# Optimization experiments

Hardware: AMD Instinct MI355X
Metric: run time of the kernel (lower is better)

The kernel has to match this reference:

```python
import jax, jax.numpy as jnp
import numpy as np

T, B, S = 32, 32, 64
I = H = C = 1024  # input_size == hidden_size required by the original module's wiring
A = 128           # attention_size


def setup_inputs() -> dict:
    key = jax.random.key(0)
    ks = jax.random.split(key, 10)
    s_ih = 1.0 / np.sqrt(H)
    s_a = 1.0 / np.sqrt(H + C)
    return {
        "inputs": jax.random.normal(ks[0], (T, B, I), jnp.float32),
        "context": jax.random.normal(ks[1], (S, B, C), jnp.float32),
        # LSTMCell params (PyTorch layout: gates ordered i, f, g, o)
        "W_ih": jax.random.normal(ks[2], (4 * H, I), jnp.float32) * s_ih,
        "W_hh": jax.random.normal(ks[3], (4 * H, H), jnp.float32) * s_ih,
        "b_ih": jax.random.normal(ks[4], (4 * H,), jnp.float32) * s_ih,
        "b_hh": jax.random.normal(ks[5], (4 * H,), jnp.float32) * s_ih,
        # Attention params: linear1 [A, H+C], linear2 [1, A]
        "W1": jax.random.normal(ks[6], (A, H + C), jnp.float32) * s_a,
        "b1": jax.random.normal(ks[7], (A,), jnp.float32) * s_a,
        "W2": jax.random.normal(ks[8], (1, A), jnp.float32) * (1.0 / np.sqrt(A)),
        "b2": jax.random.normal(ks[9], (1,), jnp.float32) * (1.0 / np.sqrt(A)),
    }


def reference(inputs, context, W_ih, W_hh, b_ih, b_hh, W1, b1, W2, b2):
    Tn, Bn, _ = inputs.shape
    Hn = W_hh.shape[1]
    xt = jnp.transpose(context, (1, 0, 2))  # [B, S, C]
    # Split linear1 weight into hidden-part and context-part so the
    # context projection can be hoisted out of the time loop (same math
    # as concatenating [y, xt] then applying linear1).
    W1_y = W1[:, :Hn]          # [A, H]
    W1_x = W1[:, Hn:]          # [A, C]
    ctx_proj = jnp.einsum('bsc,ac->bsa', xt, W1_x)  # [B, S, A]
    bias = b_ih + b_hh

    def step(carry, x_t):
        h, c = carry
        gates = x_t @ W_ih.T + h @ W_hh.T + bias   # [B, 4H]
        i, f, g, o = jnp.split(gates, 4, axis=-1)
        c_new = jax.nn.sigmoid(f) * c + jax.nn.sigmoid(i) * jnp.tanh(g)
        h_new = jax.nn.sigmoid(o) * jnp.tanh(c_new)
        # additive attention: linear1 (no nonlinearity in original) -> linear2 -> softmax
        hid = h_new[:, None, :] @ W1_y.T[None] + ctx_proj + b1  # [B, S, A]
        scores = jnp.einsum('bsa,a->bs', hid, W2[0]) + b2[0]    # [B, S]
        attn = jax.nn.softmax(scores, axis=-1)
        weighted = jnp.einsum('bs,bsc->bc', attn, xt)           # [B, C]
        return (h_new, c_new), (weighted, attn)

    h0 = jnp.zeros((Bn, Hn), inputs.dtype)
    (h, c), (outputs, attentions) = jax.lax.scan(step, (h0, h0), inputs)
    return outputs, h, c, attentions
```

## Files before the change

### kernel.cpp

```cpp
#include <hip/hip_runtime.h>

#define T_ 32
#define B_ 32
#define S_ 64
#define C_ 1024
#define H_ 1024
#define NWG 64
#define HSLOT 32768

typedef __attribute__((ext_vector_type(8))) short bf16x8;
typedef __attribute__((ext_vector_type(4))) float f32x4;

#define OUT_H   1048576
#define OUT_CC  1081344
#define OUT_AT  1114112

__device__ __forceinline__ ushort f2b(float f) {
  unsigned u = __float_as_uint(f);
  unsigned r = (u + 0x7FFFu + ((u >> 16) & 1u)) >> 16;
  return (ushort)r;
}
__device__ __forceinline__ float b2f(ushort h) {
  return __uint_as_float(((unsigned)h) << 16);
}

__global__ __launch_bounds__(256) void k_init(const float* __restrict__ inp, ushort* __restrict__ inpb,
                                              const float* __restrict__ Wih, ushort* __restrict__ Wihb,
                                              const float* __restrict__ Whh, ushort* __restrict__ Whhb,
                                              const float* __restrict__ W1, const float* __restrict__ W2,
                                              const float* __restrict__ bih, const float* __restrict__ bhh,
                                              float* __restrict__ v, float* __restrict__ bias,
                                              ushort* __restrict__ hring, unsigned* __restrict__ flags) {
  int blk = blockIdx.x, tid = threadIdx.x;
  if (blk < 4608) {
    const float* src; ushort* dst; int base;
    if (blk < 512) { src = inp; dst = inpb; base = blk; }
    else if (blk < 2560) { src = Wih; dst = Wihb; base = blk - 512; }
    else { src = Whh; dst = Whhb; base = blk - 2560; }
    size_t i = ((size_t)base * 256 + tid) * 8;
    float4 v0 = *reinterpret_cast<const float4*>(src + i);
    float4 v1 = *reinterpret_cast<const float4*>(src + i + 4);
    uint4 o;
    o.x = (unsigned)f2b(v0.x) | ((unsigned)f2b(v0.y) << 16);
    o.y = (unsigned)f2b(v0.z) | ((unsigned)f2b(v0.w) << 16);
    o.z = (unsigned)f2b(v1.x) | ((unsigned)f2b(v1.y) << 16);
    o.w = (unsigned)f2b(v1.z) | ((unsigned)f2b(v1.w) << 16);
    *reinterpret_cast<uint4*>(dst + i) = o;
  } else if (blk < 4612) {
    int c = (blk - 4608) * 256 + tid;
    float acc = 0.f;
#pragma unroll 8
    for (int a = 0; a < 128; ++a) acc += W1[a * 2048 + 1024 + c] * W2[a];
    v[c] = acc;
  } else if (blk < 4628) {
    int jj = (blk - 4612) * 256 + tid;
    bias[jj] = bih[jj] + bhh[jj];
  } else if (blk < 4632) {
    unsigned* hz = reinterpret_cast<unsigned*>(hring);
    int base = (blk - 4628) * 4096;
    for (int i = 0; i < 16; ++i) hz[base + i * 256 + tid] = 0u;
  } else {
    for (int i = 0; i < 4; ++i) flags[i * 256 + tid] = 0u;
  }
}

__global__ __launch_bounds__(1024, 4) void k_rec(const ushort* __restrict__ Whhb, const ushort* __restrict__ Wihb,
                                                 const ushort* __restrict__ inpb, ushort* __restrict__ hring,
                                                 const float* __restrict__ ctx, const float* __restrict__ v,
                                                 const float* __restrict__ bias,
                                                 float* __restrict__ out, unsigned* __restrict__ flags) {
  int tid = threadIdx.x, lane = tid & 63, w = tid >> 6;
  int wg = blockIdx.x;

  __shared__ uint4 hl4[4096];
  __shared__ float red[4][4][16][32];
  __shared__ __align__(16) ushort hs[32][16];
  __shared__ float v_s[1024];
  __shared__ float sc_s[64];
  __shared__ float att_s[64];

  if (wg >= NWG) {
    int b = wg - NWG;
    v_s[tid] = v[tid];
    __syncthreads();
    {
      int s = w * 4;
#pragma unroll
      for (int si = 0; si < 4; ++si, ++s) {
        const float* xr = ctx + (size_t)(s * B_ + b) * C_;
        float acc = 0.f;
#pragma unroll
        for (int i = 0; i < 16; ++i) { int c = lane + i * 64; acc += xr[c] * v_s[c]; }
        for (int off = 32; off; off >>= 1) acc += __shfl_down(acc, off);
        if (lane == 0) sc_s[s] = acc;
      }
    }
    __syncthreads();
    if (tid < 64) {
      float val = sc_s[tid];
      float mx = val;
      for (int off = 32; off; off >>= 1) mx = fmaxf(mx, __shfl_xor(mx, off));
      float e = expf(val - mx);
      float sm = e;
      for (int off = 32; off; off >>= 1) sm += __shfl_xor(sm, off);
      att_s[tid] = e / sm;
    }
    __syncthreads();
    if (tid < 256) {
      const float4* ctx4 = reinterpret_cast<const float4*>(ctx);
      float4 a4 = {0.f, 0.f, 0.f, 0.f};
      for (int s = 0; s < 64; ++s) {
        float a = att_s[s];
        float4 x = ctx4[(size_t)(s * B_ + b) * 256 + tid];
        a4.x += a * x.x; a4.y += a * x.y; a4.z += a * x.z; a4.w += a * x.w;
      }
#pragma unroll 4
      for (int t = 0; t < T_; ++t)
        reinterpret_cast<float4*>(out + (size_t)(t * B_ + b) * C_)[tid] = a4;
    }
    if (tid < 64) {
      float av = att_s[tid];
#pragma unroll 4
      for (int t = 0; t < T_; ++t) out[OUT_AT + (t * B_ + b) * 64 + tid] = av;
    }
    return;
  }

  int q = w & 3, ks = w >> 2;
  int g = lane >> 4, r = lane & 15;
  int hidx0 = wg * 16 + q * 4;
  int kbase = ks * 256;
  int j = (r >> 2) * 1024 + hidx0 + (r & 3);
  bf16x8 ah[8], ax[8];
  {
    const ushort* ap = Whhb + (size_t)j * 1024 + kbase + g * 8;
    const ushort* axp = Wihb + (size_t)j * 1024 + kbase + g * 8;
#pragma unroll
    for (int kk = 0; kk < 8; ++kk) {
      ah[kk] = *reinterpret_cast<const bf16x8*>(ap + kk * 32);
      ax[kk] = *reinterpret_cast<const bf16x8*>(axp + kk * 32);
    }
  }
  float c_reg = 0.f;
  int eb = tid & 31, hl = (tid >> 5) & 3, qq = tid >> 7;
  int ehidx = wg * 16 + qq * 4 + hl;
  float bs_i = 0.f, bs_f = 0.f, bs_g = 0.f, bs_o = 0.f;
  if (tid < 512) {
    bs_i = bias[ehidx];
    bs_f = bias[1024 + ehidx];
    bs_g = bias[2048 + ehidx];
    bs_o = bias[3072 + ehidx];
  }
  int cb = ks * 32 + g;

#pragma unroll 1
  for (int t = 0; t < T_; ++t) {
    {
      const uint4* s4 = reinterpret_cast<const uint4*>(inpb + (size_t)t * HSLOT);
      uint4 v0 = s4[tid], v1 = s4[tid + 1024], v2 = s4[tid + 2048], v3 = s4[tid + 3072];
      int c0 = tid, c1 = tid + 1024, c2 = tid + 2048, c3 = tid + 3072;
      hl4[(c0 >> 7) * 128 + ((c0 & 127) ^ ((c0 >> 7) & 7))] = v0;
      hl4[(c1 >> 7) * 128 + ((c1 & 127) ^ ((c1 >> 7) & 7))] = v1;
      hl4[(c2 >> 7) * 128 + ((c2 & 127) ^ ((c2 >> 7) & 7))] = v2;
      hl4[(c3 >> 7) * 128 + ((c3 & 127) ^ ((c3 >> 7) & 7))] = v3;
    }
    __syncthreads();
    f32x4 acc0 = (f32x4)(0.f), acc1 = (f32x4)(0.f);
#pragma unroll
    for (int kk = 0; kk < 8; ++kk) {
      int c16 = cb + kk * 4;
      bf16x8 b0 = *reinterpret_cast<const bf16x8*>(&hl4[r * 128 + (c16 ^ (r & 7))]);
      bf16x8 b1 = *reinterpret_cast<const bf16x8*>(&hl4[(r + 16) * 128 + (c16 ^ (r & 7))]);
      acc0 = __builtin_amdgcn_mfma_f32_16x16x32_bf16(ax[kk], b0, acc0, 0, 0, 0);
      acc1 = __builtin_amdgcn_mfma_f32_16x16x32_bf16(ax[kk], b1, acc1, 0, 0, 0);
    }
    if (t > 0 && w == 0) {
      for (;;) {
        unsigned vfl = __hip_atomic_load(&flags[lane * 16], __ATOMIC_RELAXED, __HIP_MEMORY_SCOPE_AGENT);
        if (__all((int)(vfl >= (unsigned)t))) break;
        __builtin_amdgcn_s_sleep(1);
      }
    }
    __syncthreads();
    {
      const uint4* s4 = reinterpret_cast<const uint4*>(hring + (size_t)t * HSLOT);
      uint4 v0 = s4[tid], v1 = s4[tid + 1024], v2 = s4[tid + 2048], v3 = s4[tid + 3072];
      int c0 = tid, c1 = tid + 1024, c2 = tid + 2048, c3 = tid + 3072;
      hl4[(c0 >> 7) * 128 + ((c0 & 127) ^ ((c0 >> 7) & 7))] = v0;
      hl4[(c1 >> 7) * 128 + ((c1 & 127) ^ ((c1 >> 7) & 7))] = v1;
      hl4[(c2 >> 7) * 128 + ((c2 & 127) ^ ((c2 >> 7) & 7))] = v2;
      hl4[(c3 >> 7) * 128 + ((c3 & 127) ^ ((c3 >> 7) & 7))] = v3;
    }
    __syncthreads();
#pragma unroll
    for (int kk = 0; kk < 8; ++kk) {
      int c16 = cb + kk * 4;
      bf16x8 b0 = *reinterpret_cast<const bf16x8*>(&hl4[r * 128 + (c16 ^ (r & 7))]);
      bf16x8 b1 = *reinterpret_cast<const bf16x8*>(&hl4[(r + 16) * 128 + (c16 ^ (r & 7))]);
      acc0 = __builtin_amdgcn_mfma_f32_16x16x32_bf16(ah[kk], b0, acc0, 0, 0, 0);
      acc1 = __builtin_amdgcn_mfma_f32_16x16x32_bf16(ah[kk], b1, acc1, 0, 0, 0);
    }
#pragma unroll
    for (int e = 0; e < 4; ++e) {
      red[q][ks][g * 4 + e][r] = acc0[e];
      red[q][ks][g * 4 + e][r + 16] = acc1[e];
    }
    __syncthreads();
    if (tid < 512) {
      float ig = red[qq][0][0 + hl][eb]  + red[qq][1][0 + hl][eb]  + red[qq][2][0 + hl][eb]  + red[qq][3][0 + hl][eb]  + bs_i;
      float fg = red[qq][0][4 + hl][eb]  + red[qq][1][4 + hl][eb]  + red[qq][2][4 + hl][eb]  + red[qq][3][4 + hl][eb]  + bs_f;
      float gg = red[qq][0][8 + hl][eb]  + red[qq][1][8 + hl][eb]  + red[qq][2][8 + hl][eb]  + red[qq][3][8 + hl][eb]  + bs_g;
      float og = red[qq][0][12 + hl][eb] + red[qq][1][12 + hl][eb] + red[qq][2][12 + hl][eb] + red[qq][3][12 + hl][eb] + bs_o;
      float si = 1.f / (1.f + __expf(-ig));
      float sf = 1.f / (1.f + __expf(-fg));
      float so = 1.f / (1.f + __expf(-og));
      float c_new = sf * c_reg + si * tanhf(gg);
      float h_new = so * tanhf(c_new);
      c_reg = c_new;
      hs[eb][qq * 4 + hl] = f2b(h_new);
      if (t == T_ - 1) {
        out[OUT_H + eb * 1024 + ehidx] = h_new;
        out[OUT_CC + eb * 1024 + ehidx] = c_new;
      }
    }
    __syncthreads();
    if (t != T_ - 1 && w == 0) {
      ushort* hout = hring + (size_t)(t + 1) * HSLOT;
      int b = lane >> 1, half = lane & 1;
      uint4 vv = *reinterpret_cast<const uint4*>(&hs[b][half * 8]);
      unsigned* hp = reinterpret_cast<unsigned*>(hout) + b * 512 + wg * 8 + half * 4;
      __hip_atomic_store(hp + 0, vv.x, __ATOMIC_RELAXED, __HIP_MEMORY_SCOPE_AGENT);
      __hip_atomic_store(hp + 1, vv.y, __ATOMIC_RELAXED, __HIP_MEMORY_SCOPE_AGENT);
      __hip_atomic_store(hp + 2, vv.z, __ATOMIC_RELAXED, __HIP_MEMORY_SCOPE_AGENT);
      __hip_atomic_store(hp + 3, vv.w, __ATOMIC_RELAXED, __HIP_MEMORY_SCOPE_AGENT);
      asm volatile("s_waitcnt vmcnt(0)" ::: "memory");
      if (lane == 0)
        __hip_atomic_store(&flags[wg * 16], (unsigned)(t + 1), __ATOMIC_RELAXED, __HIP_MEMORY_SCOPE_AGENT);
    }
  }
}

extern "C" void kernel_launch(void* const* d_in, const int* in_sizes, int n_in,
                              void* d_out, int out_size, void* d_ws, size_t ws_size,
                              hipStream_t stream) {
  const float* inp = (const float*)d_in[0];
  const float* ctx = (const float*)d_in[1];
  const float* Wih = (const float*)d_in[2];
  const float* Whh = (const float*)d_in[3];
  const float* bih = (const float*)d_in[4];
  const float* bhh = (const float*)d_in[5];
  const float* W1  = (const float*)d_in[6];
  const float* W2  = (const float*)d_in[8];
  float* out = (float*)d_out;
  char* wsb = (char*)d_ws;

  float* v     = (float*)(wsb + 0);
  float* bias  = (float*)(wsb + 4096);
  ushort* hring = (ushort*)(wsb + 32768);
  ushort* inpb = (ushort*)(wsb + 2195456);
  ushort* Wihb = (ushort*)(wsb + 4292608);
  ushort* Whhb = (ushort*)(wsb + 12681216);
  unsigned* flags = (unsigned*)(wsb + 21069824);

  hipLaunchKernelGGL(k_init, dim3(4633), dim3(256), 0, stream,
                     inp, inpb, Wih, Wihb, Whh, Whhb, W1, W2, bih, bhh, v, bias, hring, flags);

  const ushort* Whhb_c = Whhb;
  const ushort* Wihb_c = Wihb;
  const ushort* inpb_c = inpb;
  const float* ctx_c = ctx;
  const float* v_c = v;
  const float* bias_c = bias;
  void* kargs[9];
  kargs[0] = (void*)&Whhb_c;
  kargs[1] = (void*)&Wihb_c;
  kargs[2] = (void*)&inpb_c;
  kargs[3] = (void*)&hring;
  kargs[4] = (void*)&ctx_c;
  kargs[5] = (void*)&v_c;
  kargs[6] = (void*)&bias_c;
  kargs[7] = (void*)&out;
  kargs[8] = (void*)&flags;
  hipLaunchCooperativeKernel((const void*)k_rec, dim3(NWG + 32), dim3(1024), kargs, 0, stream);
}
```

Measured before the change: 198.0 us.

## Replicate LSTM recurrence per XCD and precompute input projection upfront

The recurrence now runs as 8 independent replicas, one per XCD, each with 32 workgroups owning 32 hidden units. Workgroups get their rank by atomically counting on the XCD id, and each replica keeps its own hidden-state ring, so per-step flag polling and h exchange stay within one XCD's L2. The x·W_ih^T projection for all timesteps is hoisted into a prologue that writes a bf16 buffer, and the weight-to-bf16 conversion moves into k_rec, which drops it from k_init. This should shorten the serial per-step critical path, at the cost of redundant recurrence work across the replicas and a dependence on the hardware scheduler placing exactly 32 blocks on each XCD.

```diff
diff --git a/kernel.cpp b/kernel.cpp
--- a/kernel.cpp
+++ b/kernel.cpp
@@ -5,8 +5,8 @@
 #define S_ 64
 #define C_ 1024
 #define H_ 1024
-#define NWG 64
 #define HSLOT 32768
+#define NXCD 8
 
 typedef __attribute__((ext_vector_type(8))) short bf16x8;
 typedef __attribute__((ext_vector_type(4))) float f32x4;
@@ -25,138 +25,209 @@
 }
 
 __global__ __launch_bounds__(256) void k_init(const float* __restrict__ inp, ushort* __restrict__ inpb,
-                                              const float* __restrict__ Wih, ushort* __restrict__ Wihb,
-                                              const float* __restrict__ Whh, ushort* __restrict__ Whhb,
                                               const float* __restrict__ W1, const float* __restrict__ W2,
                                               const float* __restrict__ bih, const float* __restrict__ bhh,
                                               float* __restrict__ v, float* __restrict__ bias,
                                               ushort* __restrict__ hring, unsigned* __restrict__ flags) {
   int blk = blockIdx.x, tid = threadIdx.x;
-  if (blk < 4608) {
-    const float* src; ushort* dst; int base;
-    if (blk < 512) { src = inp; dst = inpb; base = blk; }
-    else if (blk < 2560) { src = Wih; dst = Wihb; base = blk - 512; }
-    else { src = Whh; dst = Whhb; base = blk - 2560; }
-    size_t i = ((size_t)base * 256 + tid) * 8;
-    float4 v0 = *reinterpret_cast<const float4*>(src + i);
-    float4 v1 = *reinterpret_cast<const float4*>(src + i + 4);
+  if (blk < 512) {
+    size_t i = ((size_t)blk * 256 + tid) * 8;
+    float4 v0 = *reinterpret_cast<const float4*>(inp + i);
+    float4 v1 = *reinterpret_cast<const float4*>(inp + i + 4);
     uint4 o;
     o.x = (unsigned)f2b(v0.x) | ((unsigned)f2b(v0.y) << 16);
     o.y = (unsigned)f2b(v0.z) | ((unsigned)f2b(v0.w) << 16);
     o.z = (unsigned)f2b(v1.x) | ((unsigned)f2b(v1.y) << 16);
     o.w = (unsigned)f2b(v1.z) | ((unsigned)f2b(v1.w) << 16);
-    *reinterpret_cast<uint4*>(dst + i) = o;
-  } else if (blk < 4612) {
-    int c = (blk - 4608) * 256 + tid;
+    *reinterpret_cast<uint4*>(inpb + i) = o;
+  } else if (blk < 516) {
+    int c = (blk - 512) * 256 + tid;
     float acc = 0.f;
 #pragma unroll 8
     for (int a = 0; a < 128; ++a) acc += W1[a * 2048 + 1024 + c] * W2[a];
     v[c] = acc;
-  } else if (blk < 4628) {
-    int jj = (blk - 4612) * 256 + tid;
+  } else if (blk < 532) {
+    int jj = (blk - 516) * 256 + tid;
     bias[jj] = bih[jj] + bhh[jj];
-  } else if (blk < 4632) {
-    unsigned* hz = reinterpret_cast<unsigned*>(hring);
-    int base = (blk - 4628) * 4096;
-    for (int i = 0; i < 16; ++i) hz[base + i * 256 + tid] = 0u;
+  } else if (blk < 564) {
+    int base = (blk - 532) * 4096;
+    for (int i = 0; i < 16; ++i) {
+      int idx = base + i * 256 + tid;
+      int xcd = idx >> 14, off = idx & 16383;
+      reinterpret_cast<unsigned*>(hring + (size_t)xcd * 33 * HSLOT)[off] = 0u;
+    }
   } else {
-    for (int i = 0; i < 4; ++i) flags[i * 256 + tid] = 0u;
-  }
-}
-
-__global__ __launch_bounds__(1024, 4) void k_rec(const ushort* __restrict__ Whhb, const ushort* __restrict__ Wihb,
+    for (int i = 0; i < 17; ++i) {
+      int idx = i * 256 + tid;
+      if (idx < 4104) flags[idx] = 0u;
+    }
+  }
+}
+
+__global__ __launch_bounds__(1024, 4) void k_rec(const float* __restrict__ Wih, const float* __restrict__ Whh,
                                                  const ushort* __restrict__ inpb, ushort* __restrict__ hring,
                                                  const float* __restrict__ ctx, const float* __restrict__ v,
-                                                 const float* __restrict__ bias,
-                                                 float* __restrict__ out, unsigned* __restrict__ flags) {
+                                                 const float* __restrict__ bias, float* __restrict__ out,
+                                                 unsigned* __restrict__ flags, ushort* __restrict__ xpT) {
   int tid = threadIdx.x, lane = tid & 63, w = tid >> 6;
-  int wg = blockIdx.x;
-
   __shared__ uint4 hl4[4096];
-  __shared__ float red[4][4][16][32];
-  __shared__ __align__(16) ushort hs[32][16];
+  __shared__ float red[8][2][17][33];
   __shared__ float v_s[1024];
   __shared__ float sc_s[64];
   __shared__ float att_s[64];
-
-  if (wg >= NWG) {
-    int b = wg - NWG;
-    v_s[tid] = v[tid];
-    __syncthreads();
-    {
-      int s = w * 4;
-#pragma unroll
-      for (int si = 0; si < 4; ++si, ++s) {
-        const float* xr = ctx + (size_t)(s * B_ + b) * C_;
-        float acc = 0.f;
-#pragma unroll
-        for (int i = 0; i < 16; ++i) { int c = lane + i * 64; acc += xr[c] * v_s[c]; }
-        for (int off = 32; off; off >>= 1) acc += __shfl_down(acc, off);
-        if (lane == 0) sc_s[s] = acc;
-      }
-    }
-    __syncthreads();
-    if (tid < 64) {
-      float val = sc_s[tid];
-      float mx = val;
-      for (int off = 32; off; off >>= 1) mx = fmaxf(mx, __shfl_xor(mx, off));
-      float e = expf(val - mx);
-      float sm = e;
-      for (int off = 32; off; off >>= 1) sm += __shfl_xor(sm, off);
-      att_s[tid] = e / sm;
-    }
-    __syncthreads();
-    if (tid < 256) {
-      const float4* ctx4 = reinterpret_cast<const float4*>(ctx);
-      float4 a4 = {0.f, 0.f, 0.f, 0.f};
-      for (int s = 0; s < 64; ++s) {
-        float a = att_s[s];
-        float4 x = ctx4[(size_t)(s * B_ + b) * 256 + tid];
-        a4.x += a * x.x; a4.y += a * x.y; a4.z += a * x.z; a4.w += a * x.w;
-      }
+  __shared__ float4 wgt_s[32];
+  __shared__ unsigned rank_s;
+
+  unsigned xcd;
+  asm volatile("s_getreg_b32 %0, hwreg(HW_REG_XCC_ID)" : "=s"(xcd));
+  xcd &= 7u;
+  if (tid == 0) rank_s = atomicAdd(&flags[4096 + xcd], 1u) & 31u;
+  __syncthreads();
+  int rank = (int)rank_s;
+  int hid0 = rank * 32;
+  ushort* hring_x = hring + (size_t)xcd * 33 * HSLOT;
+
+  v_s[tid] = v[tid];
+  __syncthreads();
+  {
+    int s = w * 4;
+#pragma unroll
+    for (int si = 0; si < 4; ++si, ++s) {
+      const float* xr = ctx + (size_t)(s * B_ + rank) * C_;
+      float acc = 0.f;
+#pragma unroll
+      for (int i = 0; i < 16; ++i) { int c = lane + i * 64; acc += xr[c] * v_s[c]; }
+      for (int off = 32; off; off >>= 1) acc += __shfl_down(acc, off);
+      if (lane == 0) sc_s[s] = acc;
+    }
+  }
+  __syncthreads();
+  if (tid < 64) {
+    float val = sc_s[tid];
+    float mx = val;
+    for (int off = 32; off; off >>= 1) mx = fmaxf(mx, __shfl_xor(mx, off));
+    float e = expf(val - mx);
+    float sm = e;
+    for (int off = 32; off; off >>= 1) sm += __shfl_xor(sm, off);
+    att_s[tid] = e / sm;
+  }
+  __syncthreads();
+  if (tid < 32) {
+    const float4* ctx4 = reinterpret_cast<const float4*>(ctx);
+    float4 a4 = {0.f, 0.f, 0.f, 0.f};
+    for (int s = 0; s < 64; ++s) {
+      float a = att_s[s];
+      float4 x = ctx4[(size_t)(s * B_ + rank) * 256 + xcd * 32 + tid];
+      a4.x += a * x.x; a4.y += a * x.y; a4.z += a * x.z; a4.w += a * x.w;
+    }
+    wgt_s[tid] = a4;
+  }
+  __syncthreads();
+  {
+    int t = tid >> 5, c4 = tid & 31;
+    reinterpret_cast<float4*>(out)[(size_t)(t * B_ + rank) * 256 + xcd * 32 + c4] = wgt_s[c4];
+  }
+  if (tid < 64) {
+    float av = att_s[tid];
 #pragma unroll 4
-      for (int t = 0; t < T_; ++t)
-        reinterpret_cast<float4*>(out + (size_t)(t * B_ + b) * C_)[tid] = a4;
-    }
-    if (tid < 64) {
-      float av = att_s[tid];
-#pragma unroll 4
-      for (int t = 0; t < T_; ++t) out[OUT_AT + (t * B_ + b) * 64 + tid] = av;
-    }
-    return;
-  }
-
-  int q = w & 3, ks = w >> 2;
+    for (int t = 0; t < T_; ++t) out[OUT_AT + (t * B_ + rank) * 64 + tid] = av;
+  }
+
+  int tq = w >> 1, ks = w & 1;
   int g = lane >> 4, r = lane & 15;
-  int hidx0 = wg * 16 + q * 4;
-  int kbase = ks * 256;
-  int j = (r >> 2) * 1024 + hidx0 + (r & 3);
-  bf16x8 ah[8], ax[8];
+  int jrow = (r >> 2) * 1024 + hid0 + tq * 4 + (r & 3);
+
+  int eb = tid >> 5, ehl = tid & 31;
+  int ehidx = hid0 + ehl;
+  int etq = ehl >> 2, er = ehl & 3;
+
   {
-    const ushort* ap = Whhb + (size_t)j * 1024 + kbase + g * 8;
-    const ushort* axp = Wihb + (size_t)j * 1024 + kbase + g * 8;
-#pragma unroll
-    for (int kk = 0; kk < 8; ++kk) {
-      ah[kk] = *reinterpret_cast<const bf16x8*>(ap + kk * 32);
-      ax[kk] = *reinterpret_cast<const bf16x8*>(axp + kk * 32);
-    }
-  }
+    bf16x8 ax[16];
+    const float* ap = Wih + (size_t)jrow * 1024 + ks * 512 + g * 8;
+#pragma unroll
+    for (int kk = 0; kk < 16; ++kk) {
+      float4 f0 = *reinterpret_cast<const float4*>(ap + kk * 32);
+      float4 f1 = *reinterpret_cast<const float4*>(ap + kk * 32 + 4);
+      bf16x8 t8;
+      t8[0] = (short)f2b(f0.x); t8[1] = (short)f2b(f0.y);
+      t8[2] = (short)f2b(f0.z); t8[3] = (short)f2b(f0.w);
+      t8[4] = (short)f2b(f1.x); t8[5] = (short)f2b(f1.y);
+      t8[6] = (short)f2b(f1.z); t8[7] = (short)f2b(f1.w);
+      ax[kk] = t8;
+    }
+#pragma unroll 1
+    for (int mc = 0; mc < 32; ++mc) {
+      __syncthreads();
+      {
+        const uint4* s4 = reinterpret_cast<const uint4*>(inpb + (size_t)mc * HSLOT);
+        uint4 v0 = s4[tid], v1 = s4[tid + 1024], v2 = s4[tid + 2048], v3 = s4[tid + 3072];
+        int c0 = tid, c1 = tid + 1024, c2 = tid + 2048, c3 = tid + 3072;
+        hl4[(c0 >> 7) * 128 + ((c0 & 127) ^ ((c0 >> 7) & 7))] = v0;
+        hl4[(c1 >> 7) * 128 + ((c1 & 127) ^ ((c1 >> 7) & 7))] = v1;
+        hl4[(c2 >> 7) * 128 + ((c2 & 127) ^ ((c2 >> 7) & 7))] = v2;
+        hl4[(c3 >> 7) * 128 + ((c3 & 127) ^ ((c3 >> 7) & 7))] = v3;
+      }
+      __syncthreads();
+      f32x4 a0 = (f32x4)(0.f), a1 = (f32x4)(0.f);
+#pragma unroll
+      for (int kk = 0; kk < 16; ++kk) {
+        int c16 = ks * 64 + kk * 4 + g;
+        bf16x8 b0 = *reinterpret_cast<const bf16x8*>(&hl4[r * 128 + (c16 ^ (r & 7))]);
+        bf16x8 b1 = *reinterpret_cast<const bf16x8*>(&hl4[(r + 16) * 128 + (c16 ^ (r & 7))]);
+        a0 = __builtin_amdgcn_mfma_f32_16x16x32_bf16(ax[kk], b0, a0, 0, 0, 0);
+        a1 = __builtin_amdgcn_mfma_f32_16x16x32_bf16(ax[kk], b1, a1, 0, 0, 0);
+      }
+#pragma unroll
+      for (int e = 0; e < 4; ++e) {
+        red[tq][ks][g * 4 + e][r] = a0[e];
+        red[tq][ks][g * 4 + e][r + 16] = a1[e];
+      }
+      __syncthreads();
+      {
+        int m = mc * 32 + eb;
+        ushort4 xv;
+        xv.x = f2b(red[etq][0][er][eb]      + red[etq][1][er][eb]);
+        xv.y = f2b(red[etq][0][4 + er][eb]  + red[etq][1][4 + er][eb]);
+        xv.z = f2b(red[etq][0][8 + er][eb]  + red[etq][1][8 + er][eb]);
+        xv.w = f2b(red[etq][0][12 + er][eb] + red[etq][1][12 + er][eb]);
+        *reinterpret_cast<ushort4*>(xpT + ((size_t)m * 1024 + ehidx) * 4) = xv;
+      }
+    }
+    asm volatile("s_waitcnt vmcnt(0)" ::: "memory");
+    __syncthreads();
+  }
+
+  bf16x8 ah[16];
+  {
+    const float* ap = Whh + (size_t)jrow * 1024 + ks * 512 + g * 8;
+#pragma unroll
+    for (int kk = 0; kk < 16; ++kk) {
+      float4 f0 = *reinterpret_cast<const float4*>(ap + kk * 32);
+      float4 f1 = *reinterpret_cast<const float4*>(ap + kk * 32 + 4);
+      bf16x8 t8;
+      t8[0] = (short)f2b(f0.x); t8[1] = (short)f2b(f0.y);
+      t8[2] = (short)f2b(f0.z); t8[3] = (short)f2b(f0.w);
+      t8[4] = (short)f2b(f1.x); t8[5] = (short)f2b(f1.y);
+      t8[6] = (short)f2b(f1.z); t8[7] = (short)f2b(f1.w);
+      ah[kk] = t8;
+    }
+  }
+
+  float bs0 = bias[ehidx], bs1 = bias[1024 + ehidx], bs2 = bias[2048 + ehidx], bs3 = bias[3072 + ehidx];
   float c_reg = 0.f;
-  int eb = tid & 31, hl = (tid >> 5) & 3, qq = tid >> 7;
-  int ehidx = wg * 16 + qq * 4 + hl;
-  float bs_i = 0.f, bs_f = 0.f, bs_g = 0.f, bs_o = 0.f;
-  if (tid < 512) {
-    bs_i = bias[ehidx];
-    bs_f = bias[1024 + ehidx];
-    bs_g = bias[2048 + ehidx];
-    bs_o = bias[3072 + ehidx];
-  }
-  int cb = ks * 32 + g;
 
 #pragma unroll 1
   for (int t = 0; t < T_; ++t) {
+    if (t > 0 && w == 0) {
+      for (;;) {
+        unsigned vf = __hip_atomic_load(&flags[(xcd * 32 + (lane & 31)) * 16], __ATOMIC_RELAXED, __HIP_MEMORY_SCOPE_AGENT);
+        if (__all((int)(vf >= (unsigned)t))) break;
+        __builtin_amdgcn_s_sleep(1);
+      }
+    }
+    __syncthreads();
     {
-      const uint4* s4 = reinterpret_cast<const uint4*>(inpb + (size_t)t * HSLOT);
+      const uint4* s4 = reinterpret_cast<const uint4*>(hring_x + (size_t)t * HSLOT);
       uint4 v0 = s4[tid], v1 = s4[tid + 1024], v2 = s4[tid + 2048], v3 = s4[tid + 3072];
       int c0 = tid, c1 = tid + 1024, c2 = tid + 2048, c3 = tid + 3072;
       hl4[(c0 >> 7) * 128 + ((c0 & 127) ^ ((c0 >> 7) & 7))] = v0;
@@ -165,78 +236,45 @@
       hl4[(c3 >> 7) * 128 + ((c3 & 127) ^ ((c3 >> 7) & 7))] = v3;
     }
     __syncthreads();
-    f32x4 acc0 = (f32x4)(0.f), acc1 = (f32x4)(0.f);
-#pragma unroll
-    for (int kk = 0; kk < 8; ++kk) {
-      int c16 = cb + kk * 4;
+    f32x4 a0 = (f32x4)(0.f), a1 = (f32x4)(0.f);
+#pragma unroll
+    for (int kk = 0; kk < 16; ++kk) {
+      int c16 = ks * 64 + kk * 4 + g;
       bf16x8 b0 = *reinterpret_cast<const bf16x8*>(&hl4[r * 128 + (c16 ^ (r & 7))]);
       bf16x8 b1 = *reinterpret_cast<const bf16x8*>(&hl4[(r + 16) * 128 + (c16 ^ (r & 7))]);
-      acc0 = __builtin_amdgcn_mfma_f32_16x16x32_bf16(ax[kk], b0, acc0, 0, 0, 0);
-      acc1 = __builtin_amdgcn_mfma_f32_16x16x32_bf16(ax[kk], b1, acc1, 0, 0, 0);
-    }
-    if (t > 0 && w == 0) {
-      for (;;) {
-        unsigned vfl = __hip_atomic_load(&flags[lane * 16], __ATOMIC_RELAXED, __HIP_MEMORY_SCOPE_AGENT);
-        if (__all((int)(vfl >= (unsigned)t))) break;
-        __builtin_amdgcn_s_sleep(1);
-      }
+      a0 = __builtin_amdgcn_mfma_f32_16x16x32_bf16(ah[kk], b0, a0, 0, 0, 0);
+      a1 = __builtin_amdgcn_mfma_f32_16x16x32_bf16(ah[kk], b1, a1, 0, 0, 0);
+    }
+#pragma unroll
+    for (int e = 0; e < 4; ++e) {
+      red[tq][ks][g * 4 + e][r] = a0[e];
+      red[tq][ks][g * 4 + e][r + 16] = a1[e];
     }
     __syncthreads();
     {
-      const uint4* s4 = reinterpret_cast<const uint4*>(hring + (size_t)t * HSLOT);
-      uint4 v0 = s4[tid], v1 = s4[tid + 1024], v2 = s4[tid + 2048], v3 = s4[tid + 3072];
-      int c0 = tid, c1 = tid + 1024, c2 = tid + 2048, c3 = tid + 3072;
-      hl4[(c0 >> 7) * 128 + ((c0 & 127) ^ ((c0 >> 7) & 7))] = v0;
-      hl4[(c1 >> 7) * 128 + ((c1 & 127) ^ ((c1 >> 7) & 7))] = v1;
-      hl4[(c2 >> 7) * 128 + ((c2 & 127) ^ ((c2 >> 7) & 7))] = v2;
-      hl4[(c3 >> 7) * 128 + ((c3 & 127) ^ ((c3 >> 7) & 7))] = v3;
-    }
-    __syncthreads();
-#pragma unroll
-    for (int kk = 0; kk < 8; ++kk) {
-      int c16 = cb + kk * 4;
-      bf16x8 b0 = *reinterpret_cast<const bf16x8*>(&hl4[r * 128 + (c16 ^ (r & 7))]);
-      bf16x8 b1 = *reinterpret_cast<const bf16x8*>(&hl4[(r + 16) * 128 + (c16 ^ (r & 7))]);
-      acc0 = __builtin_amdgcn_mfma_f32_16x16x32_bf16(ah[kk], b0, acc0, 0, 0, 0);
-      acc1 = __builtin_amdgcn_mfma_f32_16x16x32_bf16(ah[kk], b1, acc1, 0, 0, 0);
-    }
-#pragma unroll
-    for (int e = 0; e < 4; ++e) {
-      red[q][ks][g * 4 + e][r] = acc0[e];
-      red[q][ks][g * 4 + e][r + 16] = acc1[e];
-    }
-    __syncthreads();
-    if (tid < 512) {
-      float ig = red[qq][0][0 + hl][eb]  + red[qq][1][0 + hl][eb]  + red[qq][2][0 + hl][eb]  + red[qq][3][0 + hl][eb]  + bs_i;
-      float fg = red[qq][0][4 + hl][eb]  + red[qq][1][4 + hl][eb]  + red[qq][2][4 + hl][eb]  + red[qq][3][4 + hl][eb]  + bs_f;
-      float gg = red[qq][0][8 + hl][eb]  + red[qq][1][8 + hl][eb]  + red[qq][2][8 + hl][eb]  + red[qq][3][8 + hl][eb]  + bs_g;
-      float og = red[qq][0][12 + hl][eb] + red[qq][1][12 + hl][eb] + red[qq][2][12 + hl][eb] + red[qq][3][12 + hl][eb] + bs_o;
+      int m = t * 32 + eb;
+      ushort4 xv = *reinterpret_cast<const ushort4*>(xpT + ((size_t)m * 1024 + ehidx) * 4);
+      float ig = red[etq][0][er][eb]      + red[etq][1][er][eb]      + b2f(xv.x) + bs0;
+      float fg = red[etq][0][4 + er][eb]  + red[etq][1][4 + er][eb]  + b2f(xv.y) + bs1;
+      float gg = red[etq][0][8 + er][eb]  + red[etq][1][8 + er][eb]  + b2f(xv.z) + bs2;
+      float og = red[etq][0][12 + er][eb] + red[etq][1][12 + er][eb] + b2f(xv.w) + bs3;
       float si = 1.f / (1.f + __expf(-ig));
       float sf = 1.f / (1.f + __expf(-fg));
       float so = 1.f / (1.f + __expf(-og));
       float c_new = sf * c_reg + si * tanhf(gg);
       float h_new = so * tanhf(c_new);
       c_reg = c_new;
-      hs[eb][qq * 4 + hl] = f2b(h_new);
-      if (t == T_ - 1) {
+      if (t < T_ - 1) {
+        hring_x[(size_t)(t + 1) * HSLOT + eb * 1024 + ehidx] = f2b(h_new);
+      } else {
         out[OUT_H + eb * 1024 + ehidx] = h_new;
         out[OUT_CC + eb * 1024 + ehidx] = c_new;
       }
     }
-    __syncthreads();
-    if (t != T_ - 1 && w == 0) {
-      ushort* hout = hring + (size_t)(t + 1) * HSLOT;
-      int b = lane >> 1, half = lane & 1;
-      uint4 vv = *reinterpret_cast<const uint4*>(&hs[b][half * 8]);
-      unsigned* hp = reinterpret_cast<unsigned*>(hout) + b * 512 + wg * 8 + half * 4;
-      __hip_atomic_store(hp + 0, vv.x, __ATOMIC_RELAXED, __HIP_MEMORY_SCOPE_AGENT);
-      __hip_atomic_store(hp + 1, vv.y, __ATOMIC_RELAXED, __HIP_MEMORY_SCOPE_AGENT);
-      __hip_atomic_store(hp + 2, vv.z, __ATOMIC_RELAXED, __HIP_MEMORY_SCOPE_AGENT);
-      __hip_atomic_store(hp + 3, vv.w, __ATOMIC_RELAXED, __HIP_MEMORY_SCOPE_AGENT);
-      asm volatile("s_waitcnt vmcnt(0)" ::: "memory");
-      if (lane == 0)
-        __hip_atomic_store(&flags[wg * 16], (unsigned)(t + 1), __ATOMIC_RELAXED, __HIP_MEMORY_SCOPE_AGENT);
-    }
+    asm volatile("s_waitcnt vmcnt(0)" ::: "memory");
+    __syncthreads();
+    if (t < T_ - 1 && w == 0 && lane == 0)
+      __hip_atomic_store(&flags[(xcd * 32 + rank) * 16], (unsigned)(t + 1), __ATOMIC_RELAXED, __HIP_MEMORY_SCOPE_AGENT);
   }
 }
 
@@ -254,26 +292,25 @@
   float* out = (float*)d_out;
   char* wsb = (char*)d_ws;
 
-  float* v     = (float*)(wsb + 0);
-  float* bias  = (float*)(wsb + 4096);
-  ushort* hring = (ushort*)(wsb + 32768);
-  ushort* inpb = (ushort*)(wsb + 2195456);
-  ushort* Wihb = (ushort*)(wsb + 4292608);
-  ushort* Whhb = (ushort*)(wsb + 12681216);
-  unsigned* flags = (unsigned*)(wsb + 21069824);
-
-  hipLaunchKernelGGL(k_init, dim3(4633), dim3(256), 0, stream,
-                     inp, inpb, Wih, Wihb, Whh, Whhb, W1, W2, bih, bhh, v, bias, hring, flags);
-
-  const ushort* Whhb_c = Whhb;
-  const ushort* Wihb_c = Wihb;
+  float* v      = (float*)(wsb + 0);
+  float* bias   = (float*)(wsb + 4096);
+  unsigned* flags = (unsigned*)(wsb + 20480);
+  ushort* inpb  = (ushort*)(wsb + 40960);
+  ushort* xpT   = (ushort*)(wsb + 2138112);
+  ushort* hring = (ushort*)(wsb + 10526720);
+
+  hipLaunchKernelGGL(k_init, dim3(565), dim3(256), 0, stream,
+                     inp, inpb, W1, W2, bih, bhh, v, bias, hring, flags);
+
+  const float* Wih_c = Wih;
+  const float* Whh_c = Whh;
   const ushort* inpb_c = inpb;
   const float* ctx_c = ctx;
   const float* v_c = v;
   const float* bias_c = bias;
-  void* kargs[9];
-  kargs[0] = (void*)&Whhb_c;
-  kargs[1] = (void*)&Wihb_c;
+  void* kargs[10];
+  kargs[0] = (void*)&Wih_c;
+  kargs[1] = (void*)&Whh_c;
   kargs[2] = (void*)&inpb_c;
   kargs[3] = (void*)&hring;
   kargs[4] = (void*)&ctx_c;
@@ -281,5 +318,6 @@
   kargs[6] = (void*)&bias_c;
   kargs[7] = (void*)&out;
   kargs[8] = (void*)&flags;
-  hipLaunchCooperativeKernel((const void*)k_rec, dim3(NWG + 32), dim3(1024), kargs, 0, stream);
-}
+  kargs[9] = (void*)&xpT;
+  hipLaunchCooperativeKernel((const void*)k_rec, dim3(256), dim3(1024), kargs, 0, stream);
+}
```

Measured after the change: 389.8 us. +96.9%, slower.

## Hoist input projection into parallel producer workgroups overlapping the recurrence

Applied to the files above, without the earlier changes.

Adds 128 extra workgroups to the cooperative kernel. Each one computes the input-to-gate projection x_t·W_ih for one (timestep, gate) pair, writes it as bf16 to a workspace buffer and bumps a per-timestep flag. The recurrent workgroups no longer run the W_ih MFMAs each step; they wait on that flag and add the precomputed values. The change also drops the W_hh bf16 pre-conversion, the attention vector precompute and the bias precompute from the init kernel, folding them into the main kernel's setup. This shortens the serial per-step critical path and the init kernel, at the cost of more resident workgroups, extra global traffic and an extra flag wait per step.

```diff
diff --git a/kernel.cpp b/kernel.cpp
--- a/kernel.cpp
+++ b/kernel.cpp
@@ -26,17 +26,12 @@
 
 __global__ __launch_bounds__(256) void k_init(const float* __restrict__ inp, ushort* __restrict__ inpb,
                                               const float* __restrict__ Wih, ushort* __restrict__ Wihb,
-                                              const float* __restrict__ Whh, ushort* __restrict__ Whhb,
-                                              const float* __restrict__ W1, const float* __restrict__ W2,
-                                              const float* __restrict__ bih, const float* __restrict__ bhh,
-                                              float* __restrict__ v, float* __restrict__ bias,
                                               ushort* __restrict__ hring, unsigned* __restrict__ flags) {
   int blk = blockIdx.x, tid = threadIdx.x;
-  if (blk < 4608) {
+  if (blk < 2560) {
     const float* src; ushort* dst; int base;
     if (blk < 512) { src = inp; dst = inpb; base = blk; }
-    else if (blk < 2560) { src = Wih; dst = Wihb; base = blk - 512; }
-    else { src = Whh; dst = Whhb; base = blk - 2560; }
+    else { src = Wih; dst = Wihb; base = blk - 512; }
     size_t i = ((size_t)base * 256 + tid) * 8;
     float4 v0 = *reinterpret_cast<const float4*>(src + i);
     float4 v1 = *reinterpret_cast<const float4*>(src + i + 4);
@@ -46,29 +41,22 @@
     o.z = (unsigned)f2b(v1.x) | ((unsigned)f2b(v1.y) << 16);
     o.w = (unsigned)f2b(v1.z) | ((unsigned)f2b(v1.w) << 16);
     *reinterpret_cast<uint4*>(dst + i) = o;
-  } else if (blk < 4612) {
-    int c = (blk - 4608) * 256 + tid;
-    float acc = 0.f;
-#pragma unroll 8
-    for (int a = 0; a < 128; ++a) acc += W1[a * 2048 + 1024 + c] * W2[a];
-    v[c] = acc;
-  } else if (blk < 4628) {
-    int jj = (blk - 4612) * 256 + tid;
-    bias[jj] = bih[jj] + bhh[jj];
-  } else if (blk < 4632) {
+  } else if (blk < 2564) {
     unsigned* hz = reinterpret_cast<unsigned*>(hring);
-    int base = (blk - 4628) * 4096;
+    int base = (blk - 2560) * 4096;
     for (int i = 0; i < 16; ++i) hz[base + i * 256 + tid] = 0u;
   } else {
-    for (int i = 0; i < 4; ++i) flags[i * 256 + tid] = 0u;
-  }
-}
-
-__global__ __launch_bounds__(1024, 4) void k_rec(const ushort* __restrict__ Whhb, const ushort* __restrict__ Wihb,
+    for (int i = 0; i < 8; ++i) flags[i * 256 + tid] = 0u;
+  }
+}
+
+__global__ __launch_bounds__(1024, 4) void k_rec(const float* __restrict__ Whh, const ushort* __restrict__ Wihb,
                                                  const ushort* __restrict__ inpb, ushort* __restrict__ hring,
-                                                 const float* __restrict__ ctx, const float* __restrict__ v,
-                                                 const float* __restrict__ bias,
-                                                 float* __restrict__ out, unsigned* __restrict__ flags) {
+                                                 const float* __restrict__ ctx,
+                                                 const float* __restrict__ W1, const float* __restrict__ W2,
+                                                 const float* __restrict__ bih, const float* __restrict__ bhh,
+                                                 float* __restrict__ out, unsigned* __restrict__ flags,
+                                                 ushort* __restrict__ xpT) {
   int tid = threadIdx.x, lane = tid & 63, w = tid >> 6;
   int wg = blockIdx.x;
 
@@ -79,9 +67,77 @@
   __shared__ float sc_s[64];
   __shared__ float att_s[64];
 
+  if (wg >= NWG + 32) {
+    int j = wg - (NWG + 32);
+    int t = j >> 2, gate = j & 3;
+    {
+      const uint4* s4 = reinterpret_cast<const uint4*>(inpb + (size_t)t * HSLOT);
+      uint4 v0 = s4[tid], v1 = s4[tid + 1024], v2 = s4[tid + 2048], v3 = s4[tid + 3072];
+      int c0 = tid, c1 = tid + 1024, c2 = tid + 2048, c3 = tid + 3072;
+      hl4[(c0 >> 7) * 128 + ((c0 & 127) ^ ((c0 >> 7) & 7))] = v0;
+      hl4[(c1 >> 7) * 128 + ((c1 & 127) ^ ((c1 >> 7) & 7))] = v1;
+      hl4[(c2 >> 7) * 128 + ((c2 & 127) ^ ((c2 >> 7) & 7))] = v2;
+      hl4[(c3 >> 7) * 128 + ((c3 & 127) ^ ((c3 >> 7) & 7))] = v3;
+    }
+    __syncthreads();
+    int g = lane >> 4, r = lane & 15;
+    f32x4 acc[2][4];
+#pragma unroll
+    for (int a = 0; a < 2; ++a)
+#pragma unroll
+      for (int b = 0; b < 4; ++b) acc[a][b] = (f32x4)(0.f);
+#pragma unroll 4
+    for (int kstep = 0; kstep < 32; ++kstep) {
+      int c16 = kstep * 4 + g;
+      bf16x8 af0 = *reinterpret_cast<const bf16x8*>(&hl4[r * 128 + (c16 ^ (r & 7))]);
+      bf16x8 af1 = *reinterpret_cast<const bf16x8*>(&hl4[(16 + r) * 128 + (c16 ^ (r & 7))]);
+#pragma unroll
+      for (int hq = 0; hq < 4; ++hq) {
+        int hid = w * 64 + hq * 16 + r;
+        bf16x8 bw = *reinterpret_cast<const bf16x8*>(Wihb + (size_t)(gate * 1024 + hid) * 1024 + kstep * 32 + g * 8);
+        acc[0][hq] = __builtin_amdgcn_mfma_f32_16x16x32_bf16(af0, bw, acc[0][hq], 0, 0, 0);
+        acc[1][hq] = __builtin_amdgcn_mfma_f32_16x16x32_bf16(af1, bw, acc[1][hq], 0, 0, 0);
+      }
+    }
+    __syncthreads();
+    {
+      ushort* xs = reinterpret_cast<ushort*>(hl4);
+      int q = lane >> 4;
+#pragma unroll
+      for (int bh = 0; bh < 2; ++bh)
+#pragma unroll
+        for (int hq = 0; hq < 4; ++hq)
+#pragma unroll
+          for (int e = 0; e < 4; ++e)
+            xs[(bh * 16 + q * 4 + e) * 1024 + w * 64 + hq * 16 + r] = f2b(acc[bh][hq][e]);
+    }
+    __syncthreads();
+    {
+      const unsigned long long* xs8 = reinterpret_cast<const unsigned long long*>(hl4);
+      int b = tid >> 5, k = tid & 31;
+      unsigned long long* dst = reinterpret_cast<unsigned long long*>(
+          xpT + ((size_t)(t * 32 + b) * 4 + gate) * 1024 + k * 32);
+#pragma unroll
+      for (int i = 0; i < 8; ++i) {
+        unsigned long long val = xs8[b * 256 + k * 8 + i];
+        __hip_atomic_store(dst + i, val, __ATOMIC_RELAXED, __HIP_MEMORY_SCOPE_AGENT);
+      }
+    }
+    asm volatile("s_waitcnt vmcnt(0)" ::: "memory");
+    __syncthreads();
+    if (tid == 0)
+      __hip_atomic_fetch_add(&flags[1024 + t], 1u, __ATOMIC_RELAXED, __HIP_MEMORY_SCOPE_AGENT);
+    return;
+  }
+
   if (wg >= NWG) {
     int b = wg - NWG;
-    v_s[tid] = v[tid];
+    {
+      float acc = 0.f;
+#pragma unroll 8
+      for (int a = 0; a < 128; ++a) acc += W1[a * 2048 + 1024 + tid] * W2[a];
+      v_s[tid] = acc;
+    }
     __syncthreads();
     {
       int s = w * 4;
@@ -131,14 +187,19 @@
   int hidx0 = wg * 16 + q * 4;
   int kbase = ks * 256;
   int j = (r >> 2) * 1024 + hidx0 + (r & 3);
-  bf16x8 ah[8], ax[8];
+  bf16x8 ah[8];
   {
-    const ushort* ap = Whhb + (size_t)j * 1024 + kbase + g * 8;
-    const ushort* axp = Wihb + (size_t)j * 1024 + kbase + g * 8;
+    const float* ap = Whh + (size_t)j * 1024 + kbase + g * 8;
 #pragma unroll
     for (int kk = 0; kk < 8; ++kk) {
-      ah[kk] = *reinterpret_cast<const bf16x8*>(ap + kk * 32);
-      ax[kk] = *reinterpret_cast<const bf16x8*>(axp + kk * 32);
+      float4 f0 = *reinterpret_cast<const float4*>(ap + kk * 32);
+      float4 f1 = *reinterpret_cast<const float4*>(ap + kk * 32 + 4);
+      bf16x8 t8;
+      t8[0] = (short)f2b(f0.x); t8[1] = (short)f2b(f0.y);
+      t8[2] = (short)f2b(f0.z); t8[3] = (short)f2b(f0.w);
+      t8[4] = (short)f2b(f1.x); t8[5] = (short)f2b(f1.y);
+      t8[6] = (short)f2b(f1.z); t8[7] = (short)f2b(f1.w);
+      ah[kk] = t8;
     }
   }
   float c_reg = 0.f;
@@ -146,42 +207,38 @@
   int ehidx = wg * 16 + qq * 4 + hl;
   float bs_i = 0.f, bs_f = 0.f, bs_g = 0.f, bs_o = 0.f;
   if (tid < 512) {
-    bs_i = bias[ehidx];
-    bs_f = bias[1024 + ehidx];
-    bs_g = bias[2048 + ehidx];
-    bs_o = bias[3072 + ehidx];
+    bs_i = bih[ehidx] + bhh[ehidx];
+    bs_f = bih[1024 + ehidx] + bhh[1024 + ehidx];
+    bs_g = bih[2048 + ehidx] + bhh[2048 + ehidx];
+    bs_o = bih[3072 + ehidx] + bhh[3072 + ehidx];
   }
   int cb = ks * 32 + g;
 
 #pragma unroll 1
   for (int t = 0; t < T_; ++t) {
-    {
-      const uint4* s4 = reinterpret_cast<const uint4*>(inpb + (size_t)t * HSLOT);
-      uint4 v0 = s4[tid], v1 = s4[tid + 1024], v2 = s4[tid + 2048], v3 = s4[tid + 3072];
-      int c0 = tid, c1 = tid + 1024, c2 = tid + 2048, c3 = tid + 3072;
-      hl4[(c0 >> 7) * 128 + ((c0 & 127) ^ ((c0 >> 7) & 7))] = v0;
-      hl4[(c1 >> 7) * 128 + ((c1 & 127) ^ ((c1 >> 7) & 7))] = v1;
-      hl4[(c2 >> 7) * 128 + ((c2 & 127) ^ ((c2 >> 7) & 7))] = v2;
-      hl4[(c3 >> 7) * 128 + ((c3 & 127) ^ ((c3 >> 7) & 7))] = v3;
-    }
-    __syncthreads();
-    f32x4 acc0 = (f32x4)(0.f), acc1 = (f32x4)(0.f);
-#pragma unroll
-    for (int kk = 0; kk < 8; ++kk) {
-      int c16 = cb + kk * 4;
-      bf16x8 b0 = *reinterpret_cast<const bf16x8*>(&hl4[r * 128 + (c16 ^ (r & 7))]);
-      bf16x8 b1 = *reinterpret_cast<const bf16x8*>(&hl4[(r + 16) * 128 + (c16 ^ (r & 7))]);
-      acc0 = __builtin_amdgcn_mfma_f32_16x16x32_bf16(ax[kk], b0, acc0, 0, 0, 0);
-      acc1 = __builtin_amdgcn_mfma_f32_16x16x32_bf16(ax[kk], b1, acc1, 0, 0, 0);
-    }
-    if (t > 0 && w == 0) {
+    if (w == 0) {
+      if (t > 0) {
+        for (;;) {
+          unsigned vfl = __hip_atomic_load(&flags[lane * 16], __ATOMIC_RELAXED, __HIP_MEMORY_SCOPE_AGENT);
+          if (__all((int)(vfl >= (unsigned)t))) break;
+          __builtin_amdgcn_s_sleep(1);
+        }
+      }
       for (;;) {
-        unsigned vfl = __hip_atomic_load(&flags[lane * 16], __ATOMIC_RELAXED, __HIP_MEMORY_SCOPE_AGENT);
-        if (__all((int)(vfl >= (unsigned)t))) break;
+        unsigned xf = __hip_atomic_load(&flags[1024 + t], __ATOMIC_RELAXED, __HIP_MEMORY_SCOPE_AGENT);
+        if (__all((int)(xf >= 4u))) break;
         __builtin_amdgcn_s_sleep(1);
       }
     }
     __syncthreads();
+    float xv_i = 0.f, xv_f = 0.f, xv_g = 0.f, xv_o = 0.f;
+    if (tid < 512) {
+      size_t base = (size_t)(t * 32 + eb) * 4096;
+      xv_i = b2f(xpT[base + ehidx]);
+      xv_f = b2f(xpT[base + 1024 + ehidx]);
+      xv_g = b2f(xpT[base + 2048 + ehidx]);
+      xv_o = b2f(xpT[base + 3072 + ehidx]);
+    }
     {
       const uint4* s4 = reinterpret_cast<const uint4*>(hring + (size_t)t * HSLOT);
       uint4 v0 = s4[tid], v1 = s4[tid + 1024], v2 = s4[tid + 2048], v3 = s4[tid + 3072];
@@ -192,6 +249,7 @@
       hl4[(c3 >> 7) * 128 + ((c3 & 127) ^ ((c3 >> 7) & 7))] = v3;
     }
     __syncthreads();
+    f32x4 acc0 = (f32x4)(0.f), acc1 = (f32x4)(0.f);
 #pragma unroll
     for (int kk = 0; kk < 8; ++kk) {
       int c16 = cb + kk * 4;
@@ -207,10 +265,10 @@
     }
     __syncthreads();
     if (tid < 512) {
-      float ig = red[qq][0][0 + hl][eb]  + red[qq][1][0 + hl][eb]  + red[qq][2][0 + hl][eb]  + red[qq][3][0 + hl][eb]  + bs_i;
-      float fg = red[qq][0][4 + hl][eb]  + red[qq][1][4 + hl][eb]  + red[qq][2][4 + hl][eb]  + red[qq][3][4 + hl][eb]  + bs_f;
-      float gg = red[qq][0][8 + hl][eb]  + red[qq][1][8 + hl][eb]  + red[qq][2][8 + hl][eb]  + red[qq][3][8 + hl][eb]  + bs_g;
-      float og = red[qq][0][12 + hl][eb] + red[qq][1][12 + hl][eb] + red[qq][2][12 + hl][eb] + red[qq][3][12 + hl][eb] + bs_o;
+      float ig = red[qq][0][0 + hl][eb]  + red[qq][1][0 + hl][eb]  + red[qq][2][0 + hl][eb]  + red[qq][3][0 + hl][eb]  + xv_i + bs_i;
+      float fg = red[qq][0][4 + hl][eb]  + red[qq][1][4 + hl][eb]  + red[qq][2][4 + hl][eb]  + red[qq][3][4 + hl][eb]  + xv_f + bs_f;
+      float gg = red[qq][0][8 + hl][eb]  + red[qq][1][8 + hl][eb]  + red[qq][2][8 + hl][eb]  + red[qq][3][8 + hl][eb]  + xv_g + bs_g;
+      float og = red[qq][0][12 + hl][eb] + red[qq][1][12 + hl][eb] + red[qq][2][12 + hl][eb] + red[qq][3][12 + hl][eb] + xv_o + bs_o;
       float si = 1.f / (1.f + __expf(-ig));
       float sf = 1.f / (1.f + __expf(-fg));
       float so = 1.f / (1.f + __expf(-og));
@@ -254,32 +312,34 @@
   float* out = (float*)d_out;
   char* wsb = (char*)d_ws;
 
-  float* v     = (float*)(wsb + 0);
-  float* bias  = (float*)(wsb + 4096);
-  ushort* hring = (ushort*)(wsb + 32768);
-  ushort* inpb = (ushort*)(wsb + 2195456);
-  ushort* Wihb = (ushort*)(wsb + 4292608);
-  ushort* Whhb = (ushort*)(wsb + 12681216);
-  unsigned* flags = (unsigned*)(wsb + 21069824);
-
-  hipLaunchKernelGGL(k_init, dim3(4633), dim3(256), 0, stream,
-                     inp, inpb, Wih, Wihb, Whh, Whhb, W1, W2, bih, bhh, v, bias, hring, flags);
-
-  const ushort* Whhb_c = Whhb;
+  unsigned* flags = (unsigned*)(wsb + 0);
+  ushort* inpb  = (ushort*)(wsb + 8192);
+  ushort* Wihb  = (ushort*)(wsb + 2105344);
+  ushort* xpT   = (ushort*)(wsb + 10493952);
+  ushort* hring = (ushort*)(wsb + 18882560);
+
+  hipLaunchKernelGGL(k_init, dim3(2565), dim3(256), 0, stream, inp, inpb, Wih, Wihb, hring, flags);
+
+  const float* Whh_c = Whh;
   const ushort* Wihb_c = Wihb;
   const ushort* inpb_c = inpb;
   const float* ctx_c = ctx;
-  const float* v_c = v;
-  const float* bias_c = bias;
-  void* kargs[9];
-  kargs[0] = (void*)&Whhb_c;
+  const float* W1_c = W1;
+  const float* W2_c = W2;
+  const float* bih_c = bih;
+  const float* bhh_c = bhh;
+  void* kargs[12];
+  kargs[0] = (void*)&Whh_c;
   kargs[1] = (void*)&Wihb_c;
   kargs[2] = (void*)&inpb_c;
   kargs[3] = (void*)&hring;
   kargs[4] = (void*)&ctx_c;
-  kargs[5] = (void*)&v_c;
-  kargs[6] = (void*)&bias_c;
-  kargs[7] = (void*)&out;
-  kargs[8] = (void*)&flags;
-  hipLaunchCooperativeKernel((const void*)k_rec, dim3(NWG + 32), dim3(1024), kargs, 0, stream);
-}
+  kargs[5] = (void*)&W1_c;
+  kargs[6] = (void*)&W2_c;
+  kargs[7] = (void*)&bih_c;
+  kargs[8] = (void*)&bhh_c;
+  kargs[9] = (void*)&out;
+  kargs[10] = (void*)&flags;
+  kargs[11] = (void*)&xpT;
+  hipLaunchCooperativeKernel((const void*)k_rec, dim3(NWG + 32 + 128), dim3(1024), kargs, 0, stream);
+}
```

New measurement: 269.9 us. 1.36x slower.
